# Optimization experiments

Measured on AMD Instinct MI355X. Metric: run time of the kernel, lower is better.

The kernel has to match this reference:

```python
import jax, jax.numpy as jnp
import numpy as np

B, N, D, L = 32, 512, 768, 4  # batch, nodes (incl. CLS at last index), in_dim==hidden_size, num_layers


def setup_inputs() -> dict:
    key = jax.random.key(0)
    ks = jax.random.split(key, 6)
    feature = jax.random.normal(ks[0], (B, N, D), jnp.float32)
    # token mask: random valid lengths, CLS node at the last index always present
    lengths = jax.random.randint(ks[1], (B,), N // 2, N)
    pmask = (jnp.arange(N)[None, :] < lengths[:, None]).astype(jnp.float32)
    pmask = pmask.at[:, -1].set(1.0)
    # L2C (learning-to-connect) bilinear gate params, one pair per layer
    Wq = jax.random.normal(ks[2], (L, D, D), jnp.float32) / np.sqrt(D)
    Wk = jax.random.normal(ks[3], (L, D, D), jnp.float32) / np.sqrt(D)
    # attention-pool projection Linear(in_dim, 1)
    proj_w = jax.random.normal(ks[4], (D,), jnp.float32) / np.sqrt(D)
    proj_b = jnp.zeros((), jnp.float32)
    return dict(pmask=pmask, feature=feature, Wq=Wq, Wk=Wk, proj_w=proj_w, proj_b=proj_b)


def reference(pmask, feature, Wq, Wk, proj_w, proj_b):
    full_adj = pmask[:, :, None] * pmask[:, None, :]        # [B,N,N]
    full_sum = jnp.sum(full_adj) + 1e-8
    p_sum = pmask.sum(-1)                                    # [B]
    scale = 1.0 / np.sqrt(D)
    preds = [feature]
    adjs, c_list, g_list = [], [], []
    total_l0 = jnp.zeros((), feature.dtype)
    for l in range(L):
        # L2C: bilinear sigmoid gate masked by full adjacency, L0-style loss = mean gate mass
        q = jnp.einsum('bnd,de->bne', feature, Wq[l])
        k = jnp.einsum('bnd,de->bne', feature, Wk[l])
        adj = jax.nn.sigmoid(jnp.einsum('bne,bme->bnm', q, k) * scale) * full_adj  # [B,N,N]
        total_l0 = total_l0 + jnp.sum(adj) / full_sum
        # sparse_statistics: CLS-row sparsity and graph-edge sparsity
        c_list.append(adj[:, -1, :-1].sum(-1) / p_sum)               # [B]
        g_list.append(adj[:, :-1, :-1].sum((-1, -2)) / p_sum ** 2)   # [B]
        adjs.append(adj)
        # symmetric degree normalization: D^-1/2 A D^-1/2 (diag bmm == row/col scaling)
        deg = adj.sum(2)                                              # [B,N]
        dis = jnp.where(deg > 0, jax.lax.rsqrt(jnp.maximum(deg, 1e-12)), 0.0)
        dis = jax.lax.stop_gradient(dis)                              # .detach() in original
        adj_n = dis[:, :, None] * adj * dis[:, None, :]
        # feature = adj_^T @ feature
        feature = jnp.einsum('bnm,bnd->bmd', adj_n, feature)
        preds.append(feature)
    pps = jnp.stack(preds, axis=2)                                    # [B,N,L+1,D]
    retain = jax.nn.sigmoid(jnp.einsum('bnld,d->bnl', pps, proj_w) + proj_b)  # [B,N,L+1]
    out = jnp.einsum('bnl,bnld->bnd', retain, pps)                    # [B,N,D]
    c_sparsity = jnp.stack(c_list, axis=-1)                           # [B,L]
    g_sparsity = jnp.stack(g_list, axis=-1)                           # [B,L]
    return (out, retain, jnp.stack(adjs, axis=-1), total_l0 / L, c_sparsity, g_sparsity)
```

## Files before the change

kernel.cpp:

```cpp
#include <hip/hip_runtime.h>

typedef short s16x8 __attribute__((ext_vector_type(8)));
typedef float f32x4 __attribute__((ext_vector_type(4)));

constexpr int BATCH = 32, NODES = 512, DIM = 768, LAYERS = 4;
constexpr float QK_SCALE = 0.03608439182435161f;

constexpr size_t OUT_OFF  = 0;
constexpr size_t RET_OFF  = (size_t)BATCH * NODES * DIM;
constexpr size_t ADJS_OFF = RET_OFF + (size_t)BATCH * NODES * (LAYERS + 1);
constexpr size_t L0_OFF   = ADJS_OFF + (size_t)BATCH * NODES * NODES * LAYERS;
constexpr size_t C_OFF    = L0_OFF + 1;
constexpr size_t G_OFF    = C_OFF + BATCH * LAYERS;

#define DEVI static __device__ __forceinline__

DEVI float bf2f(unsigned short u) {
    union { unsigned int i; float f; } v; v.i = ((unsigned int)u) << 16; return v.f;
}
DEVI unsigned short f2bf(float f) {
    union { float f; unsigned int i; } v; v.f = f;
    return (unsigned short)((v.i + 0x7FFFu + ((v.i >> 16) & 1u)) >> 16);
}
DEVI ushort4 pk4(float4 v) {
    ushort4 o; o.x = f2bf(v.x); o.y = f2bf(v.y); o.z = f2bf(v.z); o.w = f2bf(v.w); return o;
}
DEVI float sigm(float x) { return 1.0f / (1.0f + __expf(-x)); }
DEVI float deg2dis(float d) { return d > 0.f ? rsqrtf(fmaxf(d, 1e-12f)) : 0.f; }

DEVI void gload16(const unsigned short* g, unsigned short* l) {
    __builtin_amdgcn_global_load_lds(
        (const __attribute__((address_space(1))) unsigned int*)g,
        (__attribute__((address_space(3))) unsigned int*)l, 16, 0, 0);
}

template <int MODE>
__global__ __launch_bounds__(256) void gemm_nt(
    const unsigned short* __restrict__ A0, const unsigned short* __restrict__ B0,
    unsigned short* __restrict__ C0,
    int K, int lda, int ldb, int ldc,
    long sA, long sB, long sC,
    const float* __restrict__ pmask, float* __restrict__ deg,
    unsigned short* __restrict__ adjT,
    float* __restrict__ l0_acc, float* __restrict__ c_acc, float* __restrict__ g_acc,
    int layer)
{
    __shared__ __align__(16) unsigned short As[128 * 32];
    __shared__ __align__(16) unsigned short Bs[128 * 32];
    __shared__ float pmr[128];
    __shared__ float pmc[128];

    const int tid  = threadIdx.x;
    const int lane = tid & 63;
    const int wave = tid >> 6;
    const int wr = (wave >> 1) << 6;
    const int wc = (wave & 1) << 6;
    const int z = blockIdx.z;
    const int rows0 = blockIdx.x << 7;
    const int cols0 = blockIdx.y << 7;

    const unsigned short* A = A0 + (size_t)z * sA + (size_t)rows0 * lda;
    const unsigned short* Bsrc = B0 + (size_t)z * sB + (size_t)cols0 * ldb;

    f32x4 acc[4][4] = {};

    const int srow = wave * 16 + (lane >> 2);
    const int scb  = (lane & 3) << 3;
    const unsigned short* Ag = A + (size_t)srow * lda + scb;
    const unsigned short* Bg = Bsrc + (size_t)srow * ldb + scb;
    unsigned short* lA0 = &As[wave * 512];
    unsigned short* lA1 = &As[2048 + wave * 512];
    unsigned short* lB0 = &Bs[wave * 512];
    unsigned short* lB1 = &Bs[2048 + wave * 512];
    const size_t a64 = (size_t)64 * lda, b64 = (size_t)64 * ldb;

    const int mrow = lane & 15;
    const int kq   = (lane >> 4) << 3;

    for (int kt = 0; kt < K; kt += 32) {
        __syncthreads();
        gload16(Ag + kt, lA0);
        gload16(Ag + a64 + kt, lA1);
        gload16(Bg + kt, lB0);
        gload16(Bg + b64 + kt, lB1);
        __syncthreads();

        s16x8 af[4], bfr[4];
        #pragma unroll
        for (int i = 0; i < 4; ++i) {
            af[i]  = *(const s16x8*)(&As[(wr + i * 16 + mrow) * 32 + kq]);
            bfr[i] = *(const s16x8*)(&Bs[(wc + i * 16 + mrow) * 32 + kq]);
        }
        #pragma unroll
        for (int i = 0; i < 4; ++i)
            #pragma unroll
            for (int j = 0; j < 4; ++j)
                acc[i][j] = __builtin_amdgcn_mfma_f32_16x16x32_bf16(af[i], bfr[j], acc[i][j], 0, 0, 0);
    }

    const int colb = lane & 15, quad = lane >> 4;

    if constexpr (MODE != 1) {
        unsigned short* C = C0 + (size_t)z * sC;
        #pragma unroll
        for (int i = 0; i < 4; ++i) {
            const int rbase = rows0 + wr + i * 16 + (quad << 2);
            float dv[4];
            if constexpr (MODE == 2) {
                #pragma unroll
                for (int r = 0; r < 4; ++r) dv[r] = deg2dis(deg[(size_t)z * NODES + rbase + r]);
            }
            #pragma unroll
            for (int j = 0; j < 4; ++j) {
                const int cc = cols0 + wc + j * 16 + colb;
                #pragma unroll
                for (int r = 0; r < 4; ++r) {
                    float v = acc[i][j][r];
                    if constexpr (MODE == 2) v *= dv[r];
                    C[(size_t)(rbase + r) * ldc + cc] = f2bf(v);
                }
            }
        }
    } else {
        __syncthreads();
        if (tid < 128) pmr[tid] = pmask[(size_t)z * NODES + rows0 + tid];
        else if (tid < 256) pmc[tid - 128] = pmask[(size_t)z * NODES + cols0 + (tid - 128)];
        __syncthreads();

        float tot = 0.f, gs = 0.f, cs = 0.f;
        #pragma unroll
        for (int i = 0; i < 4; ++i) {
            const int nloc = wr + i * 16 + (quad << 2);
            #pragma unroll
            for (int r = 0; r < 4; ++r) {
                const int n = rows0 + nloc + r;
                const float pmn = pmr[nloc + r];
                float dp = 0.f;
                #pragma unroll
                for (int j = 0; j < 4; ++j) {
                    const int mloc = wc + j * 16 + colb;
                    const int m = cols0 + mloc;
                    float a = pmn * pmc[mloc] * sigm(acc[i][j][r] * QK_SCALE);
                    acc[i][j][r] = a;
                    dp += a;
                    tot += a;
                    if (m < NODES - 1) {
                        if (n < NODES - 1) gs += a;
                        else cs += a;
                    }
                }
                dp += __shfl_xor(dp, 1, 16);
                dp += __shfl_xor(dp, 2, 16);
                dp += __shfl_xor(dp, 4, 16);
                dp += __shfl_xor(dp, 8, 16);
                if (colb == 0) atomicAdd(&deg[(size_t)z * NODES + n], dp);
            }
        }
        #pragma unroll
        for (int i = 0; i < 4; ++i) {
            const int nb = rows0 + wr + i * 16 + (quad << 2);
            #pragma unroll
            for (int j = 0; j < 4; ++j) {
                const int m = cols0 + wc + j * 16 + colb;
                ushort4 pk;
                pk.x = f2bf(acc[i][j][0]); pk.y = f2bf(acc[i][j][1]);
                pk.z = f2bf(acc[i][j][2]); pk.w = f2bf(acc[i][j][3]);
                *(ushort4*)(adjT + ((size_t)z * NODES + m) * NODES + nb) = pk;
            }
        }
        #pragma unroll
        for (int o = 1; o < 64; o <<= 1) {
            tot += __shfl_xor(tot, o, 64);
            gs  += __shfl_xor(gs, o, 64);
            cs  += __shfl_xor(cs, o, 64);
        }
        if (lane == 0) {
            atomicAdd(l0_acc, tot);
            atomicAdd(&g_acc[z * LAYERS + layer], gs);
            atomicAdd(&c_acc[z * LAYERS + layer], cs);
        }
    }
}

__global__ __launch_bounds__(256) void interleave_adjs(
    const unsigned short* __restrict__ adjT, float* __restrict__ adjs)
{
    __shared__ unsigned short t[4][32][36];
    const int b = blockIdx.z, m0 = blockIdx.x << 5, n0 = blockIdx.y << 5;
    const int tr = threadIdx.x >> 3, tc = (threadIdx.x & 7) << 2;
    #pragma unroll
    for (int l = 0; l < LAYERS; ++l) {
        ushort4 v = *(const ushort4*)(adjT + (((size_t)l * BATCH + b) * NODES + m0 + tr) * NODES + n0 + tc);
        t[l][tr][tc] = v.x; t[l][tr][tc + 1] = v.y; t[l][tr][tc + 2] = v.z; t[l][tr][tc + 3] = v.w;
    }
    __syncthreads();
    float* dst = adjs + (((size_t)b * NODES + n0 + tr) * NODES + m0 + tc) * LAYERS;
    #pragma unroll
    for (int mm = 0; mm < 4; ++mm) {
        float4 f;
        f.x = bf2f(t[0][tc + mm][tr]); f.y = bf2f(t[1][tc + mm][tr]);
        f.z = bf2f(t[2][tc + mm][tr]); f.w = bf2f(t[3][tc + mm][tr]);
        *(float4*)(dst + mm * 4) = f;
    }
}

__global__ void fp_transpose(const unsigned short* __restrict__ X, const float* __restrict__ deg,
                             unsigned short* __restrict__ fpt)
{
    __shared__ unsigned short t[32][36];
    const int b = blockIdx.z;
    const int n0 = blockIdx.x << 5, d0 = blockIdx.y << 5;
    const int tr = threadIdx.x >> 3, tc = (threadIdx.x & 7) << 2;
    const float dv = deg2dis(deg[(size_t)b * NODES + n0 + tr]);
    ushort4 v = *(const ushort4*)(X + ((size_t)b * NODES + n0 + tr) * DIM + d0 + tc);
    t[tr][tc]     = f2bf(bf2f(v.x) * dv);
    t[tr][tc + 1] = f2bf(bf2f(v.y) * dv);
    t[tr][tc + 2] = f2bf(bf2f(v.z) * dv);
    t[tr][tc + 3] = f2bf(bf2f(v.w) * dv);
    __syncthreads();
    ushort4 o;
    o.x = t[tc + 0][tr]; o.y = t[tc + 1][tr]; o.z = t[tc + 2][tr]; o.w = t[tc + 3][tr];
    *(ushort4*)(fpt + ((size_t)b * DIM + d0 + tr) * NODES + n0 + tc) = o;
}

__global__ void cast_all(const float* __restrict__ feat, const float* __restrict__ Wq,
                         const float* __restrict__ Wk, unsigned short* __restrict__ featb,
                         unsigned short* __restrict__ Wqb, unsigned short* __restrict__ Wkb)
{
    const int bx = blockIdx.x;
    const float* src; unsigned short* dst; size_t base;
    if (bx < 12288)      { src = feat; dst = featb; base = (size_t)bx * 1024; }
    else if (bx < 14592) { src = Wq;   dst = Wqb;   base = (size_t)(bx - 12288) * 1024; }
    else                 { src = Wk;   dst = Wkb;   base = (size_t)(bx - 14592) * 1024; }
    const size_t i = base + ((size_t)threadIdx.x << 2);
    float4 v = *(const float4*)(src + i);
    *(ushort4*)(dst + i) = pk4(v);
}

__global__ void psum_kernel(const float* __restrict__ pm, float* __restrict__ ps)
{
    const int b = blockIdx.x, t = threadIdx.x;
    float s = pm[(size_t)b * NODES + t] + pm[(size_t)b * NODES + 256 + t];
    #pragma unroll
    for (int o = 1; o < 64; o <<= 1) s += __shfl_xor(s, o, 64);
    __shared__ float sh[4];
    if ((t & 63) == 0) sh[t >> 6] = s;
    __syncthreads();
    if (t == 0) ps[b] = sh[0] + sh[1] + sh[2] + sh[3];
}

__global__ __launch_bounds__(256) void final_out(
    const float* __restrict__ X0f, const unsigned short* __restrict__ X1,
    const unsigned short* __restrict__ X2, const unsigned short* __restrict__ X3,
    const unsigned short* __restrict__ X4,
    const float* __restrict__ pw, const float* __restrict__ pb,
    const float* __restrict__ ps, const float* __restrict__ c_acc,
    const float* __restrict__ g_acc, const float* __restrict__ l0,
    float* __restrict__ ob)
{
    if (blockIdx.x == 0) {
        const int t = threadIdx.x;
        if (t < BATCH * LAYERS) {
            const int b = t >> 2;
            const float p = ps[b];
            ob[C_OFF + t] = c_acc[t] / p;
            ob[G_OFF + t] = g_acc[t] / (p * p);
        }
        if (t == 0) {
            float fs = 1e-8f;
            for (int b = 0; b < BATCH; ++b) fs += ps[b] * ps[b];
            ob[L0_OFF] = l0[0] / (fs * (float)LAYERS);
        }
    }

    const int row = (blockIdx.x << 2) + (threadIdx.x >> 6);
    const int lane = threadIdx.x & 63;
    const unsigned short* Xb[4] = { X1 + (size_t)row * DIM, X2 + (size_t)row * DIM,
                                    X3 + (size_t)row * DIM, X4 + (size_t)row * DIM };
    float xs[5][12];
    float dot[5] = {};
    #pragma unroll
    for (int c = 0; c < 3; ++c) {
        const int idx = c * 256 + (lane << 2);
        float4 wv = *(const float4*)(pw + idx);
        float4 x0 = *(const float4*)(X0f + (size_t)row * DIM + idx);
        xs[0][c * 4 + 0] = x0.x; xs[0][c * 4 + 1] = x0.y;
        xs[0][c * 4 + 2] = x0.z; xs[0][c * 4 + 3] = x0.w;
        dot[0] += x0.x * wv.x + x0.y * wv.y + x0.z * wv.z + x0.w * wv.w;
        #pragma unroll
        for (int l = 0; l < 4; ++l) {
            ushort4 xv = *(const ushort4*)(Xb[l] + idx);
            float a0 = bf2f(xv.x), a1 = bf2f(xv.y), a2 = bf2f(xv.z), a3 = bf2f(xv.w);
            xs[l + 1][c * 4 + 0] = a0; xs[l + 1][c * 4 + 1] = a1;
            xs[l + 1][c * 4 + 2] = a2; xs[l + 1][c * 4 + 3] = a3;
            dot[l + 1] += a0 * wv.x + a1 * wv.y + a2 * wv.z + a3 * wv.w;
        }
    }
    #pragma unroll
    for (int l = 0; l < 5; ++l)
        #pragma unroll
        for (int o = 1; o < 64; o <<= 1) dot[l] += __shfl_xor(dot[l], o, 64);
    const float pbv = pb[0];
    float r[5];
    #pragma unroll
    for (int l = 0; l < 5; ++l) r[l] = sigm(dot[l] + pbv);
    if (lane == 0) {
        float* rr = ob + RET_OFF + (size_t)row * (LAYERS + 1);
        rr[0] = r[0]; rr[1] = r[1]; rr[2] = r[2]; rr[3] = r[3]; rr[4] = r[4];
    }
    float* orow = ob + OUT_OFF + (size_t)row * DIM;
    #pragma unroll
    for (int c = 0; c < 3; ++c) {
        float4 p;
        p.x = r[0] * xs[0][c * 4 + 0]; p.y = r[0] * xs[0][c * 4 + 1];
        p.z = r[0] * xs[0][c * 4 + 2]; p.w = r[0] * xs[0][c * 4 + 3];
        #pragma unroll
        for (int l = 1; l < 5; ++l) {
            p.x += r[l] * xs[l][c * 4 + 0]; p.y += r[l] * xs[l][c * 4 + 1];
            p.z += r[l] * xs[l][c * 4 + 2]; p.w += r[l] * xs[l][c * 4 + 3];
        }
        *(float4*)(orow + c * 256 + (lane << 2)) = p;
    }
}

extern "C" void kernel_launch(void* const* d_in, const int* in_sizes, int n_in,
                              void* d_out, int out_size, void* d_ws, size_t ws_size,
                              hipStream_t stream)
{
    (void)in_sizes; (void)n_in; (void)out_size; (void)ws_size;
    const float* pmask = (const float*)d_in[0];
    const float* feat  = (const float*)d_in[1];
    const float* Wq    = (const float*)d_in[2];
    const float* Wk    = (const float*)d_in[3];
    const float* projw = (const float*)d_in[4];
    const float* projb = (const float*)d_in[5];
    float* ob = (float*)d_out;

    char* w = (char*)d_ws;
    unsigned short* Xb[4];
    Xb[0] = (unsigned short*)(w + 0);
    Xb[1] = (unsigned short*)(w + 25165824);
    Xb[2] = (unsigned short*)(w + 50331648);
    Xb[3] = (unsigned short*)(w + 75497472);
    unsigned short* qws   = (unsigned short*)(w + 100663296);
    unsigned short* featb = (unsigned short*)(w + 125829120);
    unsigned short* adjT  = (unsigned short*)(w + 150994944);
    unsigned short* Wqb   = (unsigned short*)(w + 218103808);
    unsigned short* Wkb   = (unsigned short*)(w + 222822400);
    unsigned short* MT    = (unsigned short*)(w + 227540992);
    float* deg_all = (float*)(w + 232259584);
    float* c_acc   = (float*)(w + 232521728);
    float* g_acc   = (float*)(w + 232522240);
    float* l0_acc  = (float*)(w + 232522752);
    float* p_sum   = (float*)(w + 232523008);

    dim3 blk(256);
    hipMemsetAsync(w + 232259584, 0, 263680, stream);

    cast_all<<<dim3(16896), blk, 0, stream>>>(feat, Wq, Wk, featb, Wqb, Wkb);
    psum_kernel<<<dim3(32), blk, 0, stream>>>(pmask, p_sum);

    gemm_nt<0><<<dim3(6, 6, 4), blk, 0, stream>>>(
        Wkb, Wqb, MT, DIM, DIM, DIM, DIM,
        (long)DIM * DIM, (long)DIM * DIM, (long)DIM * DIM,
        nullptr, nullptr, nullptr, nullptr, nullptr, nullptr, 0);

    for (int l = 0; l < LAYERS; ++l) {
        float* deg_l = deg_all + (size_t)l * BATCH * NODES;
        unsigned short* adjT_l = adjT + (size_t)l * BATCH * NODES * NODES;
        const unsigned short* Xsrc = (l == 0) ? featb : Xb[l - 1];

        gemm_nt<0><<<dim3(128, 6, 1), blk, 0, stream>>>(
            Xsrc, MT + (size_t)l * DIM * DIM, qws,
            DIM, DIM, DIM, DIM, 0L, 0L, 0L,
            nullptr, nullptr, nullptr, nullptr, nullptr, nullptr, 0);

        gemm_nt<1><<<dim3(4, 4, 32), blk, 0, stream>>>(
            qws, Xsrc, nullptr,
            DIM, DIM, DIM, 0, (long)NODES * DIM, (long)NODES * DIM, 0L,
            pmask, deg_l, adjT_l, l0_acc, c_acc, g_acc, l);

        fp_transpose<<<dim3(16, 24, 32), blk, 0, stream>>>(Xsrc, deg_l, qws);

        gemm_nt<2><<<dim3(4, 6, 32), blk, 0, stream>>>(
            adjT_l, qws, Xb[l],
            NODES, NODES, NODES, DIM, (long)NODES * NODES, (long)DIM * NODES, (long)NODES * DIM,
            nullptr, deg_l, nullptr, nullptr, nullptr, nullptr, 0);
    }

    interleave_adjs<<<dim3(16, 16, 32), blk, 0, stream>>>(adjT, ob + ADJS_OFF);
    final_out<<<dim3(4096), blk, 0, stream>>>(feat, Xb[0], Xb[1], Xb[2], Xb[3],
                                              projw, projb, p_sum, c_acc, g_acc, l0_acc, ob);
}
```

Before: 835.8 us.

## Add 256x256-tile 8-wave pipelined GEMM kernel for per-layer matmuls

```diff
diff --git a/kernel.cpp b/kernel.cpp
--- a/kernel.cpp
+++ b/kernel.cpp
@@ -47,8 +47,6 @@
 {
     __shared__ __align__(16) unsigned short As[128 * 32];
     __shared__ __align__(16) unsigned short Bs[128 * 32];
-    __shared__ float pmr[128];
-    __shared__ float pmc[128];
 
     const int tid  = threadIdx.x;
     const int lane = tid & 63;
@@ -99,12 +97,193 @@
     }
 
     const int colb = lane & 15, quad = lane >> 4;
+    unsigned short* C = C0 + (size_t)z * sC;
+    #pragma unroll
+    for (int i = 0; i < 4; ++i) {
+        const int rbase = rows0 + wr + i * 16 + (quad << 2);
+        #pragma unroll
+        for (int j = 0; j < 4; ++j) {
+            const int cc = cols0 + wc + j * 16 + colb;
+            #pragma unroll
+            for (int r = 0; r < 4; ++r)
+                C[(size_t)(rbase + r) * ldc + cc] = f2bf(acc[i][j][r]);
+        }
+    }
+}
+
+template <int MODE>
+__global__ __launch_bounds__(512) void gemm256_nt(
+    const unsigned short* __restrict__ A0, const unsigned short* __restrict__ B0,
+    unsigned short* __restrict__ C0,
+    int K, int lda, int ldb, int ldc,
+    long sA, long sB, long sC,
+    const float* __restrict__ pmask, float* __restrict__ deg,
+    unsigned short* __restrict__ adjT,
+    float* __restrict__ l0_acc, float* __restrict__ c_acc, float* __restrict__ g_acc,
+    int layer)
+{
+    __shared__ __align__(16) unsigned short lds[2][2][2][8192];
+    __shared__ float pmr[256];
+    __shared__ float pmc[256];
+
+    const int tid  = threadIdx.x;
+    const int lane = tid & 63;
+    const int wave = tid >> 6;
+    const int wm   = wave >> 2;
+    const int wn   = wave & 3;
+    const int z = blockIdx.z;
+    const int rows0 = blockIdx.x << 8;
+    const int cols0 = blockIdx.y << 8;
+
+    const unsigned short* A = A0 + (size_t)z * sA;
+    const unsigned short* B = B0 + (size_t)z * sB;
+
+    if constexpr (MODE == 1) {
+        if (tid < 256) pmr[tid] = pmask[(size_t)z * NODES + rows0 + tid];
+        else pmc[tid - 256] = pmask[(size_t)z * NODES + cols0 + (tid - 256)];
+    }
+
+    const int srow  = lane >> 3;
+    const int scol8 = (lane & 7) ^ srow;
+
+    auto stage_half = [&](int T, int op, int h) {
+        const int base = (op == 0) ? rows0 : cols0;
+        const int ld   = (op == 0) ? lda : ldb;
+        const unsigned short* src = ((op == 0) ? A : B)
+            + (size_t)(base + h * 128 + wave * 8 + srow) * ld + (size_t)T * 64 + scol8 * 8;
+        unsigned short* dst = &lds[T & 1][op][h][wave * 512];
+        gload16(src, dst);
+        gload16(src + (size_t)64 * ld, dst + 4096);
+    };
+
+    const int nkt = K >> 6;
+
+    stage_half(0, 0, 0); stage_half(0, 0, 1);
+    stage_half(0, 1, 0); stage_half(0, 1, 1);
+    if (nkt > 1) {
+        stage_half(1, 0, 0);
+        asm volatile("s_waitcnt vmcnt(2)" ::: "memory");
+    } else {
+        asm volatile("s_waitcnt vmcnt(0)" ::: "memory");
+    }
+    __builtin_amdgcn_s_barrier();
+    asm volatile("" ::: "memory");
+
+    f32x4 acc[8][4] = {};
+
+    const int fr = lane & 15;
+    const int fq = lane >> 4;
+    const int xk = (fr & 7) << 4;
+    const int frow64 = fr * 64;
+    const int ka0 = ((fq * 16) ^ xk) >> 1;
+    const int ka1 = ((64 + fq * 16) ^ xk) >> 1;
+    const int brow = (wn & 1) * 4096;
+
+    for (int T = 0; T < nkt; ++T) {
+        const unsigned short* Ah = &lds[T & 1][0][wm][0];
+        const unsigned short* Bh = &lds[T & 1][1][wn >> 1][0];
+        s16x8 af[4][2], bq[4][2];
+
+        #pragma unroll
+        for (int i = 0; i < 4; ++i) {
+            af[i][0] = *(const s16x8*)(Ah + i * 1024 + frow64 + ka0);
+            af[i][1] = *(const s16x8*)(Ah + i * 1024 + frow64 + ka1);
+        }
+        #pragma unroll
+        for (int j = 0; j < 2; ++j) {
+            bq[j][0] = *(const s16x8*)(Bh + brow + j * 1024 + frow64 + ka0);
+            bq[j][1] = *(const s16x8*)(Bh + brow + j * 1024 + frow64 + ka1);
+        }
+        if (T + 1 < nkt) stage_half(T + 1, 0, 1);
+        asm volatile("" ::: "memory");
+        __builtin_amdgcn_s_barrier();
+        asm volatile("s_waitcnt lgkmcnt(0)" ::: "memory");
+        __builtin_amdgcn_sched_barrier(0);
+        __builtin_amdgcn_s_setprio(1);
+        #pragma unroll
+        for (int i = 0; i < 4; ++i)
+            #pragma unroll
+            for (int j = 0; j < 2; ++j)
+                #pragma unroll
+                for (int s = 0; s < 2; ++s)
+                    acc[i][j] = __builtin_amdgcn_mfma_f32_16x16x32_bf16(af[i][s], bq[j][s], acc[i][j], 0, 0, 0);
+        __builtin_amdgcn_s_setprio(0);
+        asm volatile("" ::: "memory");
+        __builtin_amdgcn_s_barrier();
+        asm volatile("" ::: "memory");
+
+        #pragma unroll
+        for (int j = 0; j < 2; ++j) {
+            bq[2 + j][0] = *(const s16x8*)(Bh + brow + (2 + j) * 1024 + frow64 + ka0);
+            bq[2 + j][1] = *(const s16x8*)(Bh + brow + (2 + j) * 1024 + frow64 + ka1);
+        }
+        if (T + 1 < nkt) stage_half(T + 1, 1, 0);
+        asm volatile("" ::: "memory");
+        __builtin_amdgcn_s_barrier();
+        asm volatile("s_waitcnt lgkmcnt(0)" ::: "memory");
+        __builtin_amdgcn_sched_barrier(0);
+        __builtin_amdgcn_s_setprio(1);
+        #pragma unroll
+        for (int i = 0; i < 4; ++i)
+            #pragma unroll
+            for (int j = 2; j < 4; ++j)
+                #pragma unroll
+                for (int s = 0; s < 2; ++s)
+                    acc[i][j] = __builtin_amdgcn_mfma_f32_16x16x32_bf16(af[i][s], bq[j][s], acc[i][j], 0, 0, 0);
+        __builtin_amdgcn_s_setprio(0);
+        asm volatile("" ::: "memory");
+        __builtin_amdgcn_s_barrier();
+        asm volatile("" ::: "memory");
+
+        #pragma unroll
+        for (int i = 0; i < 4; ++i) {
+            af[i][0] = *(const s16x8*)(Ah + (4 + i) * 1024 + frow64 + ka0);
+            af[i][1] = *(const s16x8*)(Ah + (4 + i) * 1024 + frow64 + ka1);
+        }
+        if (T + 1 < nkt) stage_half(T + 1, 1, 1);
+        asm volatile("" ::: "memory");
+        __builtin_amdgcn_s_barrier();
+        asm volatile("s_waitcnt lgkmcnt(0)" ::: "memory");
+        __builtin_amdgcn_sched_barrier(0);
+        __builtin_amdgcn_s_setprio(1);
+        #pragma unroll
+        for (int i = 0; i < 4; ++i)
+            #pragma unroll
+            for (int j = 2; j < 4; ++j)
+                #pragma unroll
+                for (int s = 0; s < 2; ++s)
+                    acc[4 + i][j] = __builtin_amdgcn_mfma_f32_16x16x32_bf16(af[i][s], bq[j][s], acc[4 + i][j], 0, 0, 0);
+        __builtin_amdgcn_s_setprio(0);
+        asm volatile("" ::: "memory");
+        __builtin_amdgcn_s_barrier();
+        asm volatile("" ::: "memory");
+
+        if (T + 2 < nkt) stage_half(T + 2, 0, 0);
+        asm volatile("" ::: "memory");
+        __builtin_amdgcn_s_barrier();
+        asm volatile("" ::: "memory");
+        __builtin_amdgcn_s_setprio(1);
+        #pragma unroll
+        for (int i = 0; i < 4; ++i)
+            #pragma unroll
+            for (int j = 0; j < 2; ++j)
+                #pragma unroll
+                for (int s = 0; s < 2; ++s)
+                    acc[4 + i][j] = __builtin_amdgcn_mfma_f32_16x16x32_bf16(af[i][s], bq[j][s], acc[4 + i][j], 0, 0, 0);
+        __builtin_amdgcn_s_setprio(0);
+        if (T + 2 < nkt) asm volatile("s_waitcnt vmcnt(2)" ::: "memory");
+        else             asm volatile("s_waitcnt vmcnt(0)" ::: "memory");
+        __builtin_amdgcn_s_barrier();
+        asm volatile("" ::: "memory");
+    }
+
+    const int quad4 = fq << 2;
 
     if constexpr (MODE != 1) {
         unsigned short* C = C0 + (size_t)z * sC;
         #pragma unroll
-        for (int i = 0; i < 4; ++i) {
-            const int rbase = rows0 + wr + i * 16 + (quad << 2);
+        for (int i = 0; i < 8; ++i) {
+            const int rbase = rows0 + wm * 128 + i * 16 + quad4;
             float dv[4];
             if constexpr (MODE == 2) {
                 #pragma unroll
@@ -112,7 +291,7 @@
             }
             #pragma unroll
             for (int j = 0; j < 4; ++j) {
-                const int cc = cols0 + wc + j * 16 + colb;
+                const int cc = cols0 + wn * 64 + j * 16 + fr;
                 #pragma unroll
                 for (int r = 0; r < 4; ++r) {
                     float v = acc[i][j][r];
@@ -122,15 +301,10 @@
             }
         }
     } else {
-        __syncthreads();
-        if (tid < 128) pmr[tid] = pmask[(size_t)z * NODES + rows0 + tid];
-        else if (tid < 256) pmc[tid - 128] = pmask[(size_t)z * NODES + cols0 + (tid - 128)];
-        __syncthreads();
-
         float tot = 0.f, gs = 0.f, cs = 0.f;
         #pragma unroll
-        for (int i = 0; i < 4; ++i) {
-            const int nloc = wr + i * 16 + (quad << 2);
+        for (int i = 0; i < 8; ++i) {
+            const int nloc = wm * 128 + i * 16 + quad4;
             #pragma unroll
             for (int r = 0; r < 4; ++r) {
                 const int n = rows0 + nloc + r;
@@ -138,7 +312,7 @@
                 float dp = 0.f;
                 #pragma unroll
                 for (int j = 0; j < 4; ++j) {
-                    const int mloc = wc + j * 16 + colb;
+                    const int mloc = wn * 64 + j * 16 + fr;
                     const int m = cols0 + mloc;
                     float a = pmn * pmc[mloc] * sigm(acc[i][j][r] * QK_SCALE);
                     acc[i][j][r] = a;
@@ -153,15 +327,15 @@
                 dp += __shfl_xor(dp, 2, 16);
                 dp += __shfl_xor(dp, 4, 16);
                 dp += __shfl_xor(dp, 8, 16);
-                if (colb == 0) atomicAdd(&deg[(size_t)z * NODES + n], dp);
+                if (fr == 0) atomicAdd(&deg[(size_t)z * NODES + n], dp);
             }
         }
         #pragma unroll
-        for (int i = 0; i < 4; ++i) {
-            const int nb = rows0 + wr + i * 16 + (quad << 2);
+        for (int i = 0; i < 8; ++i) {
+            const int nb = rows0 + wm * 128 + i * 16 + quad4;
             #pragma unroll
             for (int j = 0; j < 4; ++j) {
-                const int m = cols0 + wc + j * 16 + colb;
+                const int m = cols0 + wn * 64 + j * 16 + fr;
                 ushort4 pk;
                 pk.x = f2bf(acc[i][j][0]); pk.y = f2bf(acc[i][j][1]);
                 pk.z = f2bf(acc[i][j][2]); pk.w = f2bf(acc[i][j][3]);
@@ -355,6 +529,7 @@
     float* p_sum   = (float*)(w + 232523008);
 
     dim3 blk(256);
+    dim3 blk5(512);
     hipMemsetAsync(w + 232259584, 0, 263680, stream);
 
     cast_all<<<dim3(16896), blk, 0, stream>>>(feat, Wq, Wk, featb, Wqb, Wkb);
@@ -370,19 +545,19 @@
         unsigned short* adjT_l = adjT + (size_t)l * BATCH * NODES * NODES;
         const unsigned short* Xsrc = (l == 0) ? featb : Xb[l - 1];
 
-        gemm_nt<0><<<dim3(128, 6, 1), blk, 0, stream>>>(
+        gemm256_nt<0><<<dim3(64, 3, 1), blk5, 0, stream>>>(
             Xsrc, MT + (size_t)l * DIM * DIM, qws,
             DIM, DIM, DIM, DIM, 0L, 0L, 0L,
             nullptr, nullptr, nullptr, nullptr, nullptr, nullptr, 0);
 
-        gemm_nt<1><<<dim3(4, 4, 32), blk, 0, stream>>>(
+        gemm256_nt<1><<<dim3(2, 2, 32), blk5, 0, stream>>>(
             qws, Xsrc, nullptr,
             DIM, DIM, DIM, 0, (long)NODES * DIM, (long)NODES * DIM, 0L,
             pmask, deg_l, adjT_l, l0_acc, c_acc, g_acc, l);
 
         fp_transpose<<<dim3(16, 24, 32), blk, 0, stream>>>(Xsrc, deg_l, qws);
 
-        gemm_nt<2><<<dim3(4, 6, 32), blk, 0, stream>>>(
+        gemm256_nt<2><<<dim3(2, 3, 32), blk5, 0, stream>>>(
             adjT_l, qws, Xb[l],
             NODES, NODES, NODES, DIM, (long)NODES * NODES, (long)DIM * NODES, (long)NODES * DIM,
             nullptr, deg_l, nullptr, nullptr, nullptr, nullptr, 0);
```

Measured after the change: 782.6 us. 6.4% less time.
